# Optimization experiments

Measured on AMD Instinct MI355X. Metric: run time of the kernel, lower is better.

The kernel has to match this reference:

```python
import jax, jax.numpy as jnp
import numpy as np
from jax import lax

RATE = 2
KSIZE = 3
FUSE_K = 3
PAD = 1
SCALE = 10.0
ESCAPE_NAN = 1e-4
DN = ('NCHW', 'OIHW', 'NCHW')


def _patches(x, k, s, p):
    # x: [C,H,W] -> [L, C, k, k]  (matches torch pad + unfold(2).unfold(3) + permute)
    C = x.shape[0]
    pt = lax.conv_general_dilated_patches(
        x[None], (k, k), (s, s), [(p, p), (p, p)], dimension_numbers=DN)[0]
    oh, ow = pt.shape[1], pt.shape[2]
    # feature dim ordered (c, kh, kw)
    return pt.reshape(C, k, k, oh * ow).transpose(3, 0, 1, 2)


def setup_inputs() -> dict:
    key = jax.random.key(0)
    k1, k2 = jax.random.split(key)
    f = jax.random.normal(k1, (2, 128, 128, 128), dtype=jnp.float32)
    b = jax.random.normal(k2, (2, 128, 128, 128), dtype=jnp.float32)
    mask = jnp.zeros((1, 1, 128, 128), dtype=jnp.float32)
    return {"f": f, "b": b, "mask": mask}


def reference(f, b, mask):
    B, C, H, W = f.shape
    kernel = 2 * RATE  # 4
    # raw background patches (values for conv_transpose), per sample: [L, C, 4, 4]
    raw_w = jax.vmap(lambda bi: _patches(bi, kernel, RATE, PAD))(b)
    # nearest downsample by rate (torch nearest with scale 1/2 == strided slice)
    fd = f[:, :, ::RATE, ::RATE]
    bd = b[:, :, ::RATE, ::RATE]
    md = mask[:, :, ::RATE, ::RATE]
    fh, fw = fd.shape[2], fd.shape[3]
    bh, bw = bd.shape[2], bd.shape[3]
    L = bh * bw
    # matching (key) patches: [B, L, C, 3, 3]
    w = jax.vmap(lambda bi: _patches(bi, KSIZE, 1, PAD))(bd)
    # mask patches -> mm[l] = 1 where patch mean == 0 (valid background)
    m = _patches(md[0], KSIZE, 1, PAD)           # [L, 1, 3, 3]
    mm = (jnp.mean(m, axis=(1, 2, 3)) == 0.0).astype(f.dtype)[:, None, None]  # [L,1,1]

    fuse_w = jnp.eye(FUSE_K, dtype=f.dtype).reshape(1, 1, FUSE_K, FUSE_K)

    def fuse_conv(y):
        return lax.conv_general_dilated(y, fuse_w, (1, 1), [(1, 1), (1, 1)],
                                        dimension_numbers=DN)

    def one(xi, wi, rwi):
        # xi: [C,fh,fw], wi: [L,C,3,3], rwi: [L,C,4,4]
        norm = jnp.sqrt(jnp.sum(wi * wi, axis=(1, 2, 3), keepdims=True))
        wn = wi / jnp.maximum(norm, ESCAPE_NAN)
        # correlation scores (QK^T analogue): [1, L, fh, fw]
        yi = lax.conv_general_dilated(xi[None], wn, (1, 1), [(1, 1), (1, 1)],
                                      dimension_numbers=DN)
        # diagonal fuse convs, exactly mirroring the torch view/permute sequence
        yi = yi.reshape(1, 1, fh * fw, bh * bw)
        yi = fuse_conv(yi)
        yi = yi.reshape(fh, fw, bh, bw).transpose(1, 0, 3, 2).reshape(1, 1, fh * fw, bh * bw)
        yi = fuse_conv(yi)
        yi = yi.reshape(fw, fh, bw, bh).transpose(1, 0, 3, 2)  # [fh, fw, bh, bw]
        # faithful to the torch .view (plain contiguous reshape, no transpose)
        yi = yi.reshape(bh * bw, fh, fw)
        yi = yi * mm
        yi = jax.nn.softmax(yi * SCALE, axis=0) * mm
        # conv_transpose2d(yi, rwi, stride=rate, padding=1) / 4
        wt = jnp.flip(rwi, axis=(2, 3)).transpose(1, 0, 2, 3)  # [C, L, 4, 4]
        p = kernel - 1 - PAD  # 2
        out = lax.conv_general_dilated(yi[None], wt, (1, 1), [(p, p), (p, p)],
                                       lhs_dilation=(RATE, RATE),
                                       dimension_numbers=DN) / 4.0
        return out[0]  # [C, H, W]

    y = jax.vmap(one)(fd, w, raw_w)  # [B, C, H, W]
    return y
```

## Files before the change

### kernel.cpp

```cpp
#include <hip/hip_runtime.h>

#define CC 128
#define HH 128
#define WW 128
#define DH 64
#define DW 64
#define LTOT 4096
#define K0S 384
#define K2 2048
#define SCALE_F 10.0f
#define IMG ((size_t)CC * HH * WW)
#define PSTR 4104

typedef __attribute__((ext_vector_type(8))) short short8;
typedef __attribute__((ext_vector_type(4))) float f32x4;

struct Prep4 { const float* src[4]; unsigned short* dst[4]; float* ssq[4]; int lo[4]; };
struct PtrN2 { const float* ssq[2]; float* invn[2]; float* mmv[2]; };
struct PtrR2 { const float* src[2]; unsigned short* dst[2]; };

__device__ __forceinline__ unsigned short f2bf(float x) {
    union { float f; unsigned u; } v; v.f = x;
    unsigned r = v.u + 0x7fffu + ((v.u >> 16) & 1u);
    return (unsigned short)(r >> 16);
}
__device__ __forceinline__ float bf2f(unsigned short b) {
    union { unsigned u; float f; } v; v.u = ((unsigned)b) << 16;
    return v.f;
}

__device__ __forceinline__ f32x4 ld4u(const float* p) {
    f32x4 r; __builtin_memcpy(&r, p, 16); return r;
}

#define GLDS16(g, l) __builtin_amdgcn_global_load_lds( \
    (const __attribute__((address_space(1))) void*)(g), \
    (__attribute__((address_space(3))) void*)(l), 16, 0, 0)

__global__ __launch_bounds__(128) void split_ds_kernel(Prep4 P) {
    __shared__ float partial[2];
    int z = blockIdx.z;
    const float* __restrict__ src = P.src[z];
    unsigned short* __restrict__ dst = P.dst[z];
    int lo_in_seg1 = P.lo[z];
    int n = blockIdx.x;
    int c = threadIdx.x;
    int ny = n >> 6, nx = n & 63;
    float v = src[((size_t)c * HH + 2 * ny) * WW + 2 * nx];
    unsigned short hi = f2bf(v);
    unsigned short lo = f2bf(v - bf2f(hi));
    unsigned short* drow = dst + (size_t)n * K0S;
    drow[c]       = hi;
    drow[128 + c] = lo_in_seg1 ? lo : hi;
    drow[256 + c] = lo_in_seg1 ? hi : lo;

    float* ssq = P.ssq[z];
    if (ssq) {
        float s2 = v * v;
#pragma unroll
        for (int o = 32; o; o >>= 1) s2 += __shfl_xor(s2, o);
        if ((threadIdx.x & 63) == 0) partial[threadIdx.x >> 6] = s2;
        __syncthreads();
        if (threadIdx.x == 0) ssq[n] = partial[0] + partial[1];
    }
}

__global__ __launch_bounds__(256) void im2col_rawt_kernel(PtrR2 P) {
    int z = blockIdx.z;
    const float* __restrict__ src = P.src[z];
    unsigned short* __restrict__ dst = P.dst[z];
    int idx = blockIdx.x * 256 + threadIdx.x;
    int p = idx & (LTOT - 1);
    int m = idx >> 12;
    int px = p & 63, py = p >> 6;
    int ke = m & 3, kd = (m >> 2) & 3, c = m >> 4;
    int yy = 2 * py - 1 + kd, xx = 2 * px - 1 + ke;
    float v = 0.f;
    if (yy >= 0 && yy < HH && xx >= 0 && xx < WW)
        v = src[((size_t)c * HH + yy) * WW + xx];
    dst[idx] = f2bf(v);
}

__global__ void norm_mm_kernel(PtrN2 P, const float* __restrict__ mask) {
    int z = blockIdx.z;
    const float* __restrict__ ssq = P.ssq[z];
    float* __restrict__ inv_norm = P.invn[z];
    float* __restrict__ mmv = P.mmv[z];
    int p = blockIdx.x * blockDim.x + threadIdx.x;
    int px = p & 63, py = p >> 6;
    float s = 0.f, ms = 0.f;
    for (int di = -1; di <= 1; ++di)
        for (int dj = -1; dj <= 1; ++dj) {
            int y = py + di, x = px + dj;
            if (y >= 0 && y < DH && x >= 0 && x < DW) {
                s += ssq[y * 64 + x];
                ms += mask[(size_t)(2 * y) * WW + 2 * x];
            }
        }
    float n = sqrtf(s);
    if (n < 1e-4f) n = 1e-4f;
    inv_norm[p] = 1.f / n;
    mmv[p] = (ms == 0.f) ? 1.f : 0.f;
}

__global__ __launch_bounds__(256) void gemm_mfma(
    const unsigned short* __restrict__ Aop, const unsigned short* __restrict__ Bop,
    float* __restrict__ C, int M, int N, int K)
{
    __shared__ short As[128 * 64];
    __shared__ short Bs[128 * 64];
    int tid = threadIdx.x;
    int wave = tid >> 6, lane = tid & 63;
    int wm = (wave >> 1) * 64;
    int wn = (wave & 1) * 64;
    int bm = blockIdx.y * 128, bn = blockIdx.x * 128;

    int rowS = wave * 32;
    int lrow8 = lane >> 3;
    int gchunk = ((lane & 7) ^ lrow8) * 8;

    f32x4 acc[4][4] = {};

    int quad = lane >> 4;
    int r16 = lane & 15;
    int pc0 = ((quad)     ^ (r16 & 7)) * 8;
    int pc1 = ((4 + quad) ^ (r16 & 7)) * 8;

    const unsigned short* ap0 = Aop + (size_t)(bm + rowS +  0 + lrow8) * K + gchunk;
    const unsigned short* ap1 = Aop + (size_t)(bm + rowS +  8 + lrow8) * K + gchunk;
    const unsigned short* ap2 = Aop + (size_t)(bm + rowS + 16 + lrow8) * K + gchunk;
    const unsigned short* ap3 = Aop + (size_t)(bm + rowS + 24 + lrow8) * K + gchunk;
    const unsigned short* bp0 = Bop + (size_t)(bn + rowS +  0 + lrow8) * K + gchunk;
    const unsigned short* bp1 = Bop + (size_t)(bn + rowS +  8 + lrow8) * K + gchunk;
    const unsigned short* bp2 = Bop + (size_t)(bn + rowS + 16 + lrow8) * K + gchunk;
    const unsigned short* bp3 = Bop + (size_t)(bn + rowS + 24 + lrow8) * K + gchunk;
    short* lA = As + rowS * 64;
    short* lB = Bs + rowS * 64;

    for (int k0 = 0; k0 < K; k0 += 64) {
        GLDS16(ap0, lA);            GLDS16(ap1, lA + 8 * 64);
        GLDS16(ap2, lA + 16 * 64);  GLDS16(ap3, lA + 24 * 64);
        GLDS16(bp0, lB);            GLDS16(bp1, lB + 8 * 64);
        GLDS16(bp2, lB + 16 * 64);  GLDS16(bp3, lB + 24 * 64);
        ap0 += 64; ap1 += 64; ap2 += 64; ap3 += 64;
        bp0 += 64; bp1 += 64; bp2 += 64; bp3 += 64;
        __syncthreads();

        short8 a0[4], b0[4], a1[4], b1[4];
#pragma unroll
        for (int i = 0; i < 4; ++i) {
            a0[i] = *(const short8*)&As[(wm + i * 16 + r16) * 64 + pc0];
            b0[i] = *(const short8*)&Bs[(wn + i * 16 + r16) * 64 + pc0];
            a1[i] = *(const short8*)&As[(wm + i * 16 + r16) * 64 + pc1];
            b1[i] = *(const short8*)&Bs[(wn + i * 16 + r16) * 64 + pc1];
        }
#pragma unroll
        for (int i = 0; i < 4; ++i)
#pragma unroll
            for (int j = 0; j < 4; ++j) {
                acc[i][j] = __builtin_amdgcn_mfma_f32_16x16x32_bf16(a0[i], b0[j], acc[i][j], 0, 0, 0);
                acc[i][j] = __builtin_amdgcn_mfma_f32_16x16x32_bf16(a1[i], b1[j], acc[i][j], 0, 0, 0);
            }
        __syncthreads();
    }

    int col = lane & 15, rq = (lane >> 4) * 4;
#pragma unroll
    for (int i = 0; i < 4; ++i) {
#pragma unroll
        for (int r = 0; r < 4; ++r) {
            int m = bm + wm + i * 16 + rq + r;
#pragma unroll
            for (int j = 0; j < 4; ++j)
                C[(size_t)m * N + bn + wn + j * 16 + col] = acc[i][j][r];
        }
    }
}

__global__ __launch_bounds__(512, 2) void gemm_ring3(
    const unsigned short* __restrict__ Aop, const unsigned short* __restrict__ Bop,
    float* __restrict__ C, int N)
{
    constexpr int NT = 64;
    constexpr int BUFS = (128 + 256) * 64;
    __shared__ short lds[3 * BUFS];
    const int K = NT * 64;
    int tid = threadIdx.x;
    int wave = tid >> 6, lane = tid & 63;
    int wm = (wave >> 2) * 64;
    int wn = (wave & 3) * 64;
    int bm = blockIdx.y * 128, bn = blockIdx.x * 256;
    int lrow8 = lane >> 3;
    int gchunk = ((lane & 7) ^ lrow8) * 8;
    int r16 = lane & 15, quad = lane >> 4;
    int pc0 = ((quad)     ^ (r16 & 7)) * 8;
    int pc1 = ((4 + quad) ^ (r16 & 7)) * 8;

    const unsigned short* ap0 = Aop + (size_t)(bm + wave * 16 +  0 + lrow8) * K + gchunk;
    const unsigned short* ap1 = Aop + (size_t)(bm + wave * 16 +  8 + lrow8) * K + gchunk;
    const unsigned short* bp0 = Bop + (size_t)(bn + wave * 32 +  0 + lrow8) * K + gchunk;
    const unsigned short* bp1 = Bop + (size_t)(bn + wave * 32 +  8 + lrow8) * K + gchunk;
    const unsigned short* bp2 = Bop + (size_t)(bn + wave * 32 + 16 + lrow8) * K + gchunk;
    const unsigned short* bp3 = Bop + (size_t)(bn + wave * 32 + 24 + lrow8) * K + gchunk;

    f32x4 acc[4][4] = {};

#define STAGE_T(s) do { \
    short* la = lds + (s) * BUFS + (wave * 16) * 64; \
    short* lb = lds + (s) * BUFS + 128 * 64 + (wave * 32) * 64; \
    GLDS16(ap0, la); GLDS16(ap1, la + 8 * 64); \
    GLDS16(bp0, lb); GLDS16(bp1, lb + 8 * 64); \
    GLDS16(bp2, lb + 16 * 64); GLDS16(bp3, lb + 24 * 64); \
    ap0 += 64; ap1 += 64; bp0 += 64; bp1 += 64; bp2 += 64; bp3 += 64; } while (0)

    STAGE_T(0); STAGE_T(1); STAGE_T(2);
    asm volatile("s_waitcnt vmcnt(12)" ::: "memory");
    __builtin_amdgcn_s_barrier();
    asm volatile("" ::: "memory");

    int buf = 0;
#pragma unroll 1
    for (int T = 0; T < NT; ++T) {
        const short* Ab = lds + buf * BUFS;
        const short* Bb = Ab + 128 * 64;
        short8 a0[4], a1[4], b0[4], b1[4];
#pragma unroll
        for (int i = 0; i < 4; ++i) {
            a0[i] = *(const short8*)&Ab[(wm + i * 16 + r16) * 64 + pc0];
            a1[i] = *(const short8*)&Ab[(wm + i * 16 + r16) * 64 + pc1];
        }
        b0[0] = *(const short8*)&Bb[(wn + r16) * 64 + pc0];
        b1[0] = *(const short8*)&Bb[(wn + r16) * 64 + pc1];
#pragma unroll
        for (int j = 0; j < 4; ++j) {
            if (j < 3) {
                b0[j + 1] = *(const short8*)&Bb[(wn + (j + 1) * 16 + r16) * 64 + pc0];
                b1[j + 1] = *(const short8*)&Bb[(wn + (j + 1) * 16 + r16) * 64 + pc1];
                asm volatile("s_waitcnt lgkmcnt(2)" ::: "memory");
            } else {
                asm volatile("s_waitcnt lgkmcnt(0)" ::: "memory");
            }
            __builtin_amdgcn_sched_barrier(0);
            __builtin_amdgcn_s_setprio(1);
#pragma unroll
            for (int i = 0; i < 4; ++i) {
                acc[i][j] = __builtin_amdgcn_mfma_f32_16x16x32_bf16(a0[i], b0[j], acc[i][j], 0, 0, 0);
                acc[i][j] = __builtin_amdgcn_mfma_f32_16x16x32_bf16(a1[i], b1[j], acc[i][j], 0, 0, 0);
            }
            __builtin_amdgcn_s_setprio(0);
        }
        if (T + 2 < NT) { asm volatile("s_waitcnt vmcnt(6)" ::: "memory"); }
        else            { asm volatile("s_waitcnt vmcnt(0)" ::: "memory"); }
        __builtin_amdgcn_s_barrier();
        asm volatile("" ::: "memory");
        if (T + 3 < NT) STAGE_T(buf);
        buf = (buf == 2) ? 0 : buf + 1;
    }
#undef STAGE_T

    int col = lane & 15, rq = (lane >> 4) * 4;
#pragma unroll
    for (int i = 0; i < 4; ++i) {
#pragma unroll
        for (int r = 0; r < 4; ++r) {
            int m = bm + wm + i * 16 + rq + r;
#pragma unroll
            for (int j = 0; j < 4; ++j)
                C[(size_t)m * N + bn + wn + j * 16 + col] = acc[i][j][r];
        }
    }
}

__global__ __launch_bounds__(256) void stencil_norm_kernel(
    const float* __restrict__ C, const float* __restrict__ invn,
    float* __restrict__ Sg)
{
    int blk = blockIdx.x;
    int q = ((blk & 7) << 9) | (blk >> 3);
    int t = threadIdx.x;
    int qy = q >> 6, qx = q & 63;
    int chunk = t >> 2;
    int lanebase = (t & 3) << 4;
    int p0 = t << 4;

    f32x4 acc[4];
#pragma unroll
    for (int g = 0; g < 4; ++g) { acc[g][0] = acc[g][1] = acc[g][2] = acc[g][3] = 0.f; }

#pragma unroll
    for (int du = -1; du <= 1; ++du) {
        if (qy + du < 0 || qy + du > 63) continue;
        if (chunk + du < 0 || chunk + du > 63) continue;
#pragma unroll
        for (int dv = -1; dv <= 1; ++dv) {
            if (qx + dv < 0 || qx + dv > 63) continue;
            const float* rowp = C + (size_t)(q + 64 * du + dv) * LTOT + 64 * du + dv + p0;
#pragma unroll
            for (int g = 0; g < 4; ++g) {
                f32x4 lv = ld4u(rowp + 4 * g);
                if (dv == -1 && g == 0 && lanebase == 0)  lv[0] = 0.f;
                if (dv ==  1 && g == 3 && lanebase == 48) lv[3] = 0.f;
                acc[g] += lv;
            }
        }
    }
    float* orow = Sg + (size_t)q * PSTR;
#pragma unroll
    for (int g = 0; g < 4; ++g) {
        f32x4 iv = *(const f32x4*)(invn + p0 + 4 * g);
        *(f32x4*)(orow + p0 + 4 * g) = acc[g] * iv;
    }
    if (t == 0) { orow[-4] = orow[-3] = orow[-2] = orow[-1] = 0.f; }
    else if (t == 1) { orow[4096] = orow[4097] = orow[4098] = orow[4099] = 0.f; }
    if (q == 0) {
        float* gr = Sg - 4 - PSTR;
        for (int k = t; k < PSTR; k += 256) gr[k] = 0.f;
    }
    if (q == 4095) {
        float* gr = Sg - 4 + (size_t)4096 * PSTR;
        for (int k = t; k < PSTR; k += 256) gr[k] = 0.f;
    }
}

__global__ __launch_bounds__(256) void fused_conv_softmax_kernel(
    const float* __restrict__ Sg, const float* __restrict__ mmv,
    unsigned short* __restrict__ S16)
{
    __shared__ float redmax[4];
    __shared__ float redsum[4];
    int blk = blockIdx.x;
    int q = ((blk & 7) << 9) | (blk >> 3);
    int t = threadIdx.x;
    int lane = t & 63, wid = t >> 6;
    int chunk = t >> 2;
    int lanebase = (t & 3) << 4;
    int c0 = t << 4;

    int rbase = ((q & 63) << 6) | (q >> 6);

    f32x4 sacc[4];
#pragma unroll
    for (int g = 0; g < 4; ++g) { sacc[g][0] = sacc[g][1] = sacc[g][2] = sacc[g][3] = 0.f; }

#pragma unroll
    for (int j = 0; j < 3; ++j) {
        int r2 = rbase + (j - 1);
        if (r2 < 0 || r2 >= LTOT) continue;
        int rr = ((r2 & 63) << 6) | (r2 >> 6);
        int cj = chunk + (j - 1);
        int ccb;
        if (cj < 0)       ccb = 4031 + lanebase;
        else if (cj > 63) ccb = lanebase + 1;
        else              ccb = (cj << 6) + lanebase;
        const float* pr = Sg + (size_t)rr * PSTR + ccb;
#pragma unroll
        for (int g = 0; g < 4; ++g) {
            const float* pg = pr + 4 * g;
            f32x4 lm = ld4u(pg - (PSTR + 1));
            f32x4 l0 = ld4u(pg);
            f32x4 lp = ld4u(pg + (PSTR + 1));
            f32x4 tj = lm + l0 + lp;
            if (j == 0 && g == 0 && t == 0)   tj[0] = 0.f;
            if (j == 2 && g == 3 && t == 255) tj[3] = 0.f;
            sacc[g] += tj;
        }
    }

    float v[16];
#pragma unroll
    for (int g = 0; g < 4; ++g) {
        f32x4 m4 = *(const f32x4*)(mmv + c0 + 4 * g);
#pragma unroll
        for (int e = 0; e < 4; ++e)
            v[4 * g + e] = sacc[g][e] * m4[e] * SCALE_F;
    }
#pragma unroll
    for (int k = 0; k < 16; ++k) asm volatile("" : "+v"(v[k]));

    float mx = v[0];
#pragma unroll
    for (int i = 1; i < 16; ++i) mx = fmaxf(mx, v[i]);
#pragma unroll
    for (int o = 32; o; o >>= 1) mx = fmaxf(mx, __shfl_xor(mx, o));
    if (lane == 0) redmax[wid] = mx;
    __syncthreads();
    float gmx = fmaxf(fmaxf(redmax[0], redmax[1]), fmaxf(redmax[2], redmax[3]));

    float s = 0.f;
#pragma unroll
    for (int i = 0; i < 16; ++i) {
        v[i] = __expf(v[i] - gmx);
        s += v[i];
    }
#pragma unroll
    for (int o = 32; o; o >>= 1) s += __shfl_xor(s, o);
    if (lane == 0) redsum[wid] = s;
    __syncthreads();
    float inv = 1.f / (redsum[0] + redsum[1] + redsum[2] + redsum[3]);

    unsigned short* orow = S16 + (size_t)q * LTOT + c0;
    short8 h0, h1;
#pragma unroll
    for (int e = 0; e < 8; ++e) {
        h0[e] = (short)f2bf(v[e]     * inv * mmv[c0 + e]);
        h1[e] = (short)f2bf(v[8 + e] * inv * mmv[c0 + 8 + e]);
    }
    *(short8*)orow = h0;
    *(short8*)(orow + 8) = h1;
}

__global__ void output_kernel(const float* __restrict__ C2t, float* __restrict__ out) {
    int idx = blockIdx.x * blockDim.x + threadIdx.x;
    int x = idx & 127;
    int y = (idx >> 7) & 127;
    int c = idx >> 14;
    int oylo = max(0, (y - 1) >> 1), oyhi = min(63, (y + 1) >> 1);
    int oxlo = max(0, (x - 1) >> 1), oxhi = min(63, (x + 1) >> 1);
    float s = 0.f;
    for (int oy = oylo; oy <= oyhi; ++oy)
        for (int ox = oxlo; ox <= oxhi; ++ox) {
            int kd = y - 2 * oy + 1;
            int ke = x - 2 * ox + 1;
            s += C2t[(size_t)(c * 16 + kd * 4 + ke) * LTOT + oy * 64 + ox];
        }
    out[idx] = s * 0.25f;
}

extern "C" void kernel_launch(void* const* d_in, const int* in_sizes, int n_in,
                              void* d_out, int out_size, void* d_ws, size_t ws_size,
                              hipStream_t stream) {
    (void)in_sizes; (void)n_in; (void)out_size; (void)ws_size;
    const float* f    = (const float*)d_in[0];
    const float* b    = (const float*)d_in[1];
    const float* mask = (const float*)d_in[2];
    float* out = (float*)d_out;

    const size_t SZ_MAT  = (size_t)LTOT * LTOT * 4;
    const size_t SZ_SPAD = (size_t)PSTR * 4098 * 4;
    const size_t SZ_WR   = (size_t)K2 * LTOT * 2;
    const size_t SZ_SP   = (size_t)LTOT * K0S * 2;
    const size_t SZ_V    = (size_t)LTOT * 4;

    auto pad = [](size_t n) { return (n + 255) & ~(size_t)255; };
    char* p = (char*)d_ws;
    auto take = [&](size_t n) -> void* { void* r = (void*)p; p += pad(n); return r; };

    take(256);
    float* Buf1 = (float*)take(SZ_MAT);
    float* Spad = (float*)take(SZ_SPAD);
    unsigned short* W = (unsigned short*)take(SZ_WR);
    unsigned short* Bsp0 = (unsigned short*)take(SZ_SP);
    unsigned short* Fsp0 = (unsigned short*)take(SZ_SP);
    unsigned short* Bsp1 = (unsigned short*)take(SZ_SP);
    unsigned short* Fsp1 = (unsigned short*)take(SZ_SP);
    float* ssq0 = (float*)take(SZ_V);  float* ssq1 = (float*)take(SZ_V);
    float* invn0 = (float*)take(SZ_V); float* invn1 = (float*)take(SZ_V);
    float* mmv0 = (float*)take(SZ_V);  float* mmv1 = (float*)take(SZ_V);

    const float* f0 = f,  *b0 = b;
    const float* f1 = f + IMG, *b1 = b + IMG;

    float* Sg = Spad + PSTR + 4;
    unsigned short* S16 = (unsigned short*)Buf1;
    float* C2t = Spad;

    Prep4 P{{b0, f0, b1, f1}, {Bsp0, Fsp0, Bsp1, Fsp1},
            {ssq0, nullptr, ssq1, nullptr}, {1, 0, 1, 0}};
    split_ds_kernel<<<dim3(LTOT, 1, 4), 128, 0, stream>>>(P);
    PtrN2 nm{{ssq0, ssq1}, {invn0, invn1}, {mmv0, mmv1}};
    norm_mm_kernel<<<dim3(16, 1, 2), 256, 0, stream>>>(nm, mask);

    for (int bi = 0; bi < 2; ++bi) {
        const unsigned short* Fsp = bi ? Fsp1 : Fsp0;
        const unsigned short* Bsp = bi ? Bsp1 : Bsp0;
        const float* invn = bi ? invn1 : invn0;
        const float* mmv  = bi ? mmv1 : mmv0;

        PtrR2 rw{{bi ? b1 : b0, nullptr}, {W, nullptr}};
        im2col_rawt_kernel<<<dim3((size_t)K2 * LTOT / 256, 1, 1), 256, 0, stream>>>(rw);

        gemm_mfma<<<dim3(32, 32), 256, 0, stream>>>(Fsp, Bsp, Buf1, LTOT, LTOT, K0S);

        stencil_norm_kernel<<<LTOT, 256, 0, stream>>>(Buf1, invn, Sg);

        fused_conv_softmax_kernel<<<LTOT, 256, 0, stream>>>(Sg, mmv, S16);

        gemm_ring3<<<dim3(LTOT / 256, K2 / 128), 512, 0, stream>>>(W, S16, C2t, LTOT);

        output_kernel<<<CC * HH * WW / 256, 256, 0, stream>>>(C2t, out + (size_t)bi * IMG);
    }
}
```

Before: 518.6 us.

## Use 256x256 tiles with split-K=2 for second GEMM, sum partials in output

Replaces the 128x256 three-stage ring GEMM with a 256x256-tile kernel that splits K into two halves across blockIdx.z and double-buffers LDS. Each half writes its own FP32 partial matrix, and output_kernel now reads and adds both partials while it gathers. The larger tile raises reuse per LDS load and keeps the block count at 256. In exchange it doubles the FP32 intermediate traffic, needs twice the C2t workspace, and waits on vmcnt(0) every iteration, which shortens the load/compute overlap.

```diff
diff --git a/kernel.cpp b/kernel.cpp
--- a/kernel.cpp
+++ b/kernel.cpp
@@ -8,6 +8,8 @@
 #define LTOT 4096
 #define K0S 384
 #define K2 2048
+#define GK 4096
+#define GKH 2048
 #define SCALE_F 10.0f
 #define IMG ((size_t)CC * HH * WW)
 #define PSTR 4104
@@ -177,44 +179,49 @@
     }
 }
 
-__global__ __launch_bounds__(512, 2) void gemm_ring3(
+__global__ __launch_bounds__(512, 2) void gemm_k2(
     const unsigned short* __restrict__ Aop, const unsigned short* __restrict__ Bop,
-    float* __restrict__ C, int N)
+    float* __restrict__ Cpart)
 {
-    constexpr int NT = 64;
-    constexpr int BUFS = (128 + 256) * 64;
-    __shared__ short lds[3 * BUFS];
-    const int K = NT * 64;
+    constexpr int NT = 32;
+    constexpr int BUFS = 512 * 64;
+    __shared__ short lds[2 * BUFS];
     int tid = threadIdx.x;
     int wave = tid >> 6, lane = tid & 63;
-    int wm = (wave >> 2) * 64;
+    int wm = (wave >> 2) * 128;
     int wn = (wave & 3) * 64;
-    int bm = blockIdx.y * 128, bn = blockIdx.x * 256;
+    int bm = blockIdx.y * 256, bn = blockIdx.x * 256;
+    int ks = blockIdx.z;
     int lrow8 = lane >> 3;
     int gchunk = ((lane & 7) ^ lrow8) * 8;
     int r16 = lane & 15, quad = lane >> 4;
     int pc0 = ((quad)     ^ (r16 & 7)) * 8;
     int pc1 = ((4 + quad) ^ (r16 & 7)) * 8;
 
-    const unsigned short* ap0 = Aop + (size_t)(bm + wave * 16 +  0 + lrow8) * K + gchunk;
-    const unsigned short* ap1 = Aop + (size_t)(bm + wave * 16 +  8 + lrow8) * K + gchunk;
-    const unsigned short* bp0 = Bop + (size_t)(bn + wave * 32 +  0 + lrow8) * K + gchunk;
-    const unsigned short* bp1 = Bop + (size_t)(bn + wave * 32 +  8 + lrow8) * K + gchunk;
-    const unsigned short* bp2 = Bop + (size_t)(bn + wave * 32 + 16 + lrow8) * K + gchunk;
-    const unsigned short* bp3 = Bop + (size_t)(bn + wave * 32 + 24 + lrow8) * K + gchunk;
-
-    f32x4 acc[4][4] = {};
-
-#define STAGE_T(s) do { \
-    short* la = lds + (s) * BUFS + (wave * 16) * 64; \
-    short* lb = lds + (s) * BUFS + 128 * 64 + (wave * 32) * 64; \
-    GLDS16(ap0, la); GLDS16(ap1, la + 8 * 64); \
-    GLDS16(bp0, lb); GLDS16(bp1, lb + 8 * 64); \
-    GLDS16(bp2, lb + 16 * 64); GLDS16(bp3, lb + 24 * 64); \
-    ap0 += 64; ap1 += 64; bp0 += 64; bp1 += 64; bp2 += 64; bp3 += 64; } while (0)
-
-    STAGE_T(0); STAGE_T(1); STAGE_T(2);
-    asm volatile("s_waitcnt vmcnt(12)" ::: "memory");
+    const size_t ko = (size_t)ks * GKH + gchunk;
+    const unsigned short* ap0 = Aop + (size_t)(bm + wave * 32 +  0 + lrow8) * GK + ko;
+    const unsigned short* ap1 = Aop + (size_t)(bm + wave * 32 +  8 + lrow8) * GK + ko;
+    const unsigned short* ap2 = Aop + (size_t)(bm + wave * 32 + 16 + lrow8) * GK + ko;
+    const unsigned short* ap3 = Aop + (size_t)(bm + wave * 32 + 24 + lrow8) * GK + ko;
+    const unsigned short* bp0 = Bop + (size_t)(bn + wave * 32 +  0 + lrow8) * GK + ko;
+    const unsigned short* bp1 = Bop + (size_t)(bn + wave * 32 +  8 + lrow8) * GK + ko;
+    const unsigned short* bp2 = Bop + (size_t)(bn + wave * 32 + 16 + lrow8) * GK + ko;
+    const unsigned short* bp3 = Bop + (size_t)(bn + wave * 32 + 24 + lrow8) * GK + ko;
+
+    f32x4 acc[8][4] = {};
+
+#define STAGE2(s) do { \
+    short* la = lds + (s) * BUFS + (wave * 32) * 64; \
+    short* lb = lds + (s) * BUFS + 256 * 64 + (wave * 32) * 64; \
+    GLDS16(ap0, la);            GLDS16(ap1, la + 8 * 64); \
+    GLDS16(ap2, la + 16 * 64);  GLDS16(ap3, la + 24 * 64); \
+    GLDS16(bp0, lb);            GLDS16(bp1, lb + 8 * 64); \
+    GLDS16(bp2, lb + 16 * 64);  GLDS16(bp3, lb + 24 * 64); \
+    ap0 += 64; ap1 += 64; ap2 += 64; ap3 += 64; \
+    bp0 += 64; bp1 += 64; bp2 += 64; bp3 += 64; } while (0)
+
+    STAGE2(0); STAGE2(1);
+    asm volatile("s_waitcnt vmcnt(8)" ::: "memory");
     __builtin_amdgcn_s_barrier();
     asm volatile("" ::: "memory");
 
@@ -222,20 +229,20 @@
 #pragma unroll 1
     for (int T = 0; T < NT; ++T) {
         const short* Ab = lds + buf * BUFS;
-        const short* Bb = Ab + 128 * 64;
-        short8 a0[4], a1[4], b0[4], b1[4];
-#pragma unroll
-        for (int i = 0; i < 4; ++i) {
-            a0[i] = *(const short8*)&Ab[(wm + i * 16 + r16) * 64 + pc0];
-            a1[i] = *(const short8*)&Ab[(wm + i * 16 + r16) * 64 + pc1];
-        }
-        b0[0] = *(const short8*)&Bb[(wn + r16) * 64 + pc0];
-        b1[0] = *(const short8*)&Bb[(wn + r16) * 64 + pc1];
+        const short* Bb = Ab + 256 * 64;
+        short8 a0[8], a1[8], b0[4], b1[4];
 #pragma unroll
         for (int j = 0; j < 4; ++j) {
-            if (j < 3) {
-                b0[j + 1] = *(const short8*)&Bb[(wn + (j + 1) * 16 + r16) * 64 + pc0];
-                b1[j + 1] = *(const short8*)&Bb[(wn + (j + 1) * 16 + r16) * 64 + pc1];
+            b0[j] = *(const short8*)&Bb[(wn + j * 16 + r16) * 64 + pc0];
+            b1[j] = *(const short8*)&Bb[(wn + j * 16 + r16) * 64 + pc1];
+        }
+        a0[0] = *(const short8*)&Ab[(wm + r16) * 64 + pc0];
+        a1[0] = *(const short8*)&Ab[(wm + r16) * 64 + pc1];
+#pragma unroll
+        for (int i = 0; i < 8; ++i) {
+            if (i < 7) {
+                a0[i + 1] = *(const short8*)&Ab[(wm + (i + 1) * 16 + r16) * 64 + pc0];
+                a1[i + 1] = *(const short8*)&Ab[(wm + (i + 1) * 16 + r16) * 64 + pc1];
                 asm volatile("s_waitcnt lgkmcnt(2)" ::: "memory");
             } else {
                 asm volatile("s_waitcnt lgkmcnt(0)" ::: "memory");
@@ -243,30 +250,30 @@
             __builtin_amdgcn_sched_barrier(0);
             __builtin_amdgcn_s_setprio(1);
 #pragma unroll
-            for (int i = 0; i < 4; ++i) {
+            for (int j = 0; j < 4; ++j) {
                 acc[i][j] = __builtin_amdgcn_mfma_f32_16x16x32_bf16(a0[i], b0[j], acc[i][j], 0, 0, 0);
                 acc[i][j] = __builtin_amdgcn_mfma_f32_16x16x32_bf16(a1[i], b1[j], acc[i][j], 0, 0, 0);
             }
             __builtin_amdgcn_s_setprio(0);
         }
-        if (T + 2 < NT) { asm volatile("s_waitcnt vmcnt(6)" ::: "memory"); }
-        else            { asm volatile("s_waitcnt vmcnt(0)" ::: "memory"); }
+        asm volatile("s_waitcnt vmcnt(0)" ::: "memory");
         __builtin_amdgcn_s_barrier();
         asm volatile("" ::: "memory");
-        if (T + 3 < NT) STAGE_T(buf);
-        buf = (buf == 2) ? 0 : buf + 1;
-    }
-#undef STAGE_T
-
+        if (T + 2 < NT) STAGE2(buf);
+        buf ^= 1;
+    }
+#undef STAGE2
+
+    float* Cout = Cpart + (size_t)ks * K2 * LTOT;
     int col = lane & 15, rq = (lane >> 4) * 4;
 #pragma unroll
-    for (int i = 0; i < 4; ++i) {
+    for (int i = 0; i < 8; ++i) {
 #pragma unroll
         for (int r = 0; r < 4; ++r) {
             int m = bm + wm + i * 16 + rq + r;
 #pragma unroll
             for (int j = 0; j < 4; ++j)
-                C[(size_t)m * N + bn + wn + j * 16 + col] = acc[i][j][r];
+                Cout[(size_t)m * LTOT + bn + wn + j * 16 + col] = acc[i][j][r];
         }
     }
 }
@@ -410,6 +417,7 @@
 }
 
 __global__ void output_kernel(const float* __restrict__ C2t, float* __restrict__ out) {
+    const float* __restrict__ P1 = C2t + (size_t)K2 * LTOT;
     int idx = blockIdx.x * blockDim.x + threadIdx.x;
     int x = idx & 127;
     int y = (idx >> 7) & 127;
@@ -421,7 +429,8 @@
         for (int ox = oxlo; ox <= oxhi; ++ox) {
             int kd = y - 2 * oy + 1;
             int ke = x - 2 * ox + 1;
-            s += C2t[(size_t)(c * 16 + kd * 4 + ke) * LTOT + oy * 64 + ox];
+            size_t off = (size_t)(c * 16 + kd * 4 + ke) * LTOT + oy * 64 + ox;
+            s += C2t[off] + P1[off];
         }
     out[idx] = s * 0.25f;
 }
@@ -485,7 +494,7 @@
 
         fused_conv_softmax_kernel<<<LTOT, 256, 0, stream>>>(Sg, mmv, S16);
 
-        gemm_ring3<<<dim3(LTOT / 256, K2 / 128), 512, 0, stream>>>(W, S16, C2t, LTOT);
+        gemm_k2<<<dim3(LTOT / 256, K2 / 256, 2), 512, 0, stream>>>(W, S16, C2t);
 
         output_kernel<<<CC * HH * WW / 256, 256, 0, stream>>>(C2t, out + (size_t)bi * IMG);
     }
```

After: 512.4 us. About the same (-1.2%).
